# Kernel tuning notes

Hardware: AMD Instinct MI355X
Metric: run time of the kernel (lower is better)

## Reference

```python
import jax, jax.numpy as jnp
import numpy as np

B, S, D, E = 8, 4096, 2048, 8
CHUNK = 128
TAU = 0.7


def setup_inputs() -> dict:
    key = jax.random.key(0)
    k0, k1, k2 = jax.random.split(key, 3)
    H = D // 2
    x = jax.random.normal(k0, (B, S, D), dtype=jnp.float32)
    W1 = jax.random.normal(k1, (D, H), dtype=jnp.float32) * (1.0 / np.sqrt(D))
    b1 = jnp.zeros((H,), dtype=jnp.float32)
    W2 = jax.random.normal(k2, (H, E), dtype=jnp.float32) * (1.0 / np.sqrt(H))
    b2 = jnp.zeros((E,), dtype=jnp.float32)
    return {"x": x, "W1": W1, "b1": b1, "W2": W2, "b2": b2}


def reference(x, W1, b1, W2, b2):
    b, s, d = x.shape
    e = W2.shape[1]
    c = s // CHUNK  # num_chunks (seq_len divisible by chunk_size)
    # router MLP: Linear -> ReLU -> Linear
    logits = jnp.maximum(x @ W1 + b1, 0.0) @ W2 + b2  # [B,S,E]
    # per-chunk mean logits
    chunk_logits = logits.reshape(b, c, CHUNK, e).mean(axis=2)  # [B,C,E]
    bidx = jnp.arange(b)
    # chunk 0: plain argmax
    init = jnp.argmax(chunk_logits[:, 0], axis=-1)  # [B]
    # chunks 1..C-1: hysteresis recurrence via scan
    def step(prev, cl):  # cl: [B,E]
        ce = jnp.argmax(cl, axis=-1)
        diff = cl[bidx, ce] - cl[bidx, prev]
        new = jnp.where(diff > TAU, ce, prev)
        return new, new
    _, rest = jax.lax.scan(step, init, jnp.swapaxes(chunk_logits[:, 1:], 0, 1))
    expert_indices = jnp.concatenate([init[:, None], rest.T], axis=1)  # [B,C]
    oh = jax.nn.one_hot(expert_indices, e, dtype=logits.dtype)  # [B,C,E]
    routing_weights = jnp.broadcast_to(oh[:, :, None, :], (b, c, CHUNK, e)).reshape(b, s, e)
    return routing_weights, expert_indices
```

## Files before the change

kernel.cpp:

```cpp
#include <hip/hip_runtime.h>

typedef unsigned int uint;
typedef unsigned short ushort;

#define BB 8
#define SS 4096
#define DD 2048
#define HH 1024
#define EE 8
#define CHUNK 128
#define NCHUNK 32
#define TAU 0.7f

#define BM 128
#define BN 128
#define BK 32
#define KITERS (DD / BK)

typedef short bf16x8 __attribute__((ext_vector_type(8)));
typedef float f32x16 __attribute__((ext_vector_type(16)));

__device__ inline uint pack_hi(float a, float b) {
    return (__float_as_uint(a) >> 16) | (__float_as_uint(b) & 0xFFFF0000u);
}
__device__ inline float hi_part(float a) {
    return __uint_as_float(__float_as_uint(a) & 0xFFFF0000u);
}

__global__ __launch_bounds__(256) void reorder_w1_kernel(
    const float* __restrict__ W1, ushort* __restrict__ w1hi, ushort* __restrict__ w1lo)
{
    const int kg = blockIdx.x >> 2;
    const int n  = ((blockIdx.x & 3) << 8) + threadIdx.x;
    float v[8];
#pragma unroll
    for (int j = 0; j < 8; ++j) v[j] = W1[(size_t)(kg * 8 + j) * HH + n];
    uint hi[4], lo[4];
#pragma unroll
    for (int p = 0; p < 4; ++p) {
        const float a = v[2 * p], b = v[2 * p + 1];
        hi[p] = pack_hi(a, b);
        lo[p] = pack_hi(a - hi_part(a), b - hi_part(b));
    }
    const size_t off = (size_t)kg * HH + n;
    ((uint4*)w1hi)[off] = make_uint4(hi[0], hi[1], hi[2], hi[3]);
    ((uint4*)w1lo)[off] = make_uint4(lo[0], lo[1], lo[2], lo[3]);
}

__global__ __launch_bounds__(256, 2) void router_gemm_kernel(
    const float* __restrict__ x,
    const ushort* __restrict__ w1hi,
    const ushort* __restrict__ w1lo,
    const float* __restrict__ b1,
    const float* __restrict__ W2,
    float* __restrict__ chunk_logits)
{
    const int slice = blockIdx.x;
    const int bc    = blockIdx.y;
    const int n0    = slice * BN;

    const int tid  = threadIdx.x;
    const int wave = tid >> 6;
    const int lane = tid & 63;
    const int lm   = lane & 31;
    const int kq   = lane >> 5;
    const int wm   = (wave & 1) * 64;
    const int wn   = (wave >> 1) * 64;

    __shared__ ushort As_hi[4][BM][8];
    __shared__ ushort As_lo[4][BM][8];
    __shared__ ushort Bs_hi[4][BN][8];
    __shared__ ushort Bs_lo[4][BN][8];
    __shared__ float  W2s[BN][EE];
    __shared__ float  b1s[BN];
    __shared__ float  red[4][EE];

    const float* xrow = x + (size_t)bc * CHUNK * DD;

    ((float4*)&W2s[0][0])[tid] = ((const float4*)(W2 + (size_t)n0 * EE))[tid];
    if (tid < BN / 4) ((float4*)b1s)[tid] = ((const float4*)(b1 + n0))[tid];

    f32x16 acc[2][2];
#pragma unroll
    for (int i = 0; i < 2; ++i)
#pragma unroll
        for (int j = 0; j < 2; ++j)
#pragma unroll
            for (int r = 0; r < 16; ++r) acc[i][j][r] = 0.0f;

    const int am = tid >> 1;
    const int ah = tid & 1;

    for (int it = 0; it < KITERS; ++it) {
        const int k0 = it * BK;
        __syncthreads();

        {
            const int kgg = (k0 >> 3) + wave;
#pragma unroll
            for (int h = 0; h < 2; ++h) {
                const size_t goff = ((size_t)kgg * HH + n0 + h * 64 + lane) * 8;
                __builtin_amdgcn_global_load_lds(
                    (const __attribute__((address_space(1))) uint*)(w1hi + goff),
                    (__attribute__((address_space(3))) uint*)&Bs_hi[wave][h * 64 + lane][0],
                    16, 0, 0);
                __builtin_amdgcn_global_load_lds(
                    (const __attribute__((address_space(1))) uint*)(w1lo + goff),
                    (__attribute__((address_space(3))) uint*)&Bs_lo[wave][h * 64 + lane][0],
                    16, 0, 0);
            }
        }

        {
            const float* src = xrow + (size_t)am * DD + k0 + ah * 16;
            float4 v0 = ((const float4*)src)[0];
            float4 v1 = ((const float4*)src)[1];
            float4 v2 = ((const float4*)src)[2];
            float4 v3 = ((const float4*)src)[3];
            const float f[16] = {v0.x, v0.y, v0.z, v0.w, v1.x, v1.y, v1.z, v1.w,
                                 v2.x, v2.y, v2.z, v2.w, v3.x, v3.y, v3.z, v3.w};
            uint hi[8], lo[8];
#pragma unroll
            for (int p = 0; p < 8; ++p) {
                const float a = f[2 * p], b = f[2 * p + 1];
                hi[p] = pack_hi(a, b);
                lo[p] = pack_hi(a - hi_part(a), b - hi_part(b));
            }
            const int kg0 = ah * 2;
            *(uint4*)&As_hi[kg0][am][0]     = make_uint4(hi[0], hi[1], hi[2], hi[3]);
            *(uint4*)&As_hi[kg0 + 1][am][0] = make_uint4(hi[4], hi[5], hi[6], hi[7]);
            *(uint4*)&As_lo[kg0][am][0]     = make_uint4(lo[0], lo[1], lo[2], lo[3]);
            *(uint4*)&As_lo[kg0 + 1][am][0] = make_uint4(lo[4], lo[5], lo[6], lo[7]);
        }

        __syncthreads();

#pragma unroll
        for (int s = 0; s < 2; ++s) {
            const int kg = 2 * s + kq;
            bf16x8 a_h[2], a_l[2], b_h[2], b_l[2];
#pragma unroll
            for (int i = 0; i < 2; ++i) {
                a_h[i] = *(const bf16x8*)&As_hi[kg][wm + i * 32 + lm][0];
                a_l[i] = *(const bf16x8*)&As_lo[kg][wm + i * 32 + lm][0];
            }
#pragma unroll
            for (int j = 0; j < 2; ++j) {
                b_h[j] = *(const bf16x8*)&Bs_hi[kg][wn + j * 32 + lm][0];
                b_l[j] = *(const bf16x8*)&Bs_lo[kg][wn + j * 32 + lm][0];
            }
#pragma unroll
            for (int i = 0; i < 2; ++i)
#pragma unroll
                for (int j = 0; j < 2; ++j) {
                    acc[i][j] = __builtin_amdgcn_mfma_f32_32x32x16_bf16(
                        a_l[i], b_h[j], acc[i][j], 0, 0, 0);
                    acc[i][j] = __builtin_amdgcn_mfma_f32_32x32x16_bf16(
                        a_h[i], b_l[j], acc[i][j], 0, 0, 0);
                    acc[i][j] = __builtin_amdgcn_mfma_f32_32x32x16_bf16(
                        a_h[i], b_h[j], acc[i][j], 0, 0, 0);
                }
        }
    }

    float part[EE];
#pragma unroll
    for (int e = 0; e < EE; ++e) part[e] = 0.0f;

#pragma unroll
    for (int j = 0; j < 2; ++j) {
        const int hl = wn + j * 32 + lm;
        const float bias = b1s[hl];
        float w2r[EE];
#pragma unroll
        for (int e = 0; e < EE; ++e) w2r[e] = W2s[hl][e];
#pragma unroll
        for (int i = 0; i < 2; ++i)
#pragma unroll
            for (int r = 0; r < 16; ++r) {
                const float hv = fmaxf(acc[i][j][r] + bias, 0.0f);
#pragma unroll
                for (int e = 0; e < EE; ++e) part[e] = fmaf(hv, w2r[e], part[e]);
            }
    }

#pragma unroll
    for (int off = 32; off >= 1; off >>= 1)
#pragma unroll
        for (int e = 0; e < EE; ++e) part[e] += __shfl_down(part[e], off, 64);

    if (lane == 0)
#pragma unroll
        for (int e = 0; e < EE; ++e) red[wave][e] = part[e];
    __syncthreads();
    if (tid < EE) {
        const float s = red[0][tid] + red[1][tid] + red[2][tid] + red[3][tid];
        atomicAdd(&chunk_logits[(size_t)bc * EE + tid], s * (1.0f / CHUNK));
    }
}

__global__ void hysteresis_kernel(const float* __restrict__ chunk_logits,
                                  const float* __restrict__ b2,
                                  int* __restrict__ eidx_ws,
                                  float* __restrict__ out_idx)
{
    __shared__ float cls[BB * NCHUNK * EE];
    const int tid = threadIdx.x;
#pragma unroll
    for (int i = 0; i < 8; ++i)
        ((float4*)cls)[tid + i * 64] = ((const float4*)chunk_logits)[tid + i * 64];
    __syncthreads();

    const int b = tid;
    if (b >= BB) return;
    float b2r[EE];
#pragma unroll
    for (int e = 0; e < EE; ++e) b2r[e] = b2[e];

    const float* cl = cls + b * NCHUNK * EE;
    int prev = 0;
    for (int c = 0; c < NCHUNK; ++c) {
        float v[EE];
        float best = -3.4e38f;
        int ce = 0;
#pragma unroll
        for (int e = 0; e < EE; ++e) {
            const float lv = cl[c * EE + e] + b2r[e];
            v[e] = lv;
            if (lv > best) { best = lv; ce = e; }
        }
        if (c == 0) prev = ce;
        else if (best - v[prev] > TAU) prev = ce;
        eidx_ws[b * NCHUNK + c] = prev;
        out_idx[b * NCHUNK + c] = (float)prev;
    }
}

__global__ __launch_bounds__(256) void onehot_kernel(const int* __restrict__ eidx,
                                                     float* __restrict__ out)
{
    const int tok = blockIdx.x * blockDim.x + threadIdx.x;
    if (tok >= BB * SS) return;
    const int b = tok / SS;
    const int s = tok - b * SS;
    const int idx = eidx[b * NCHUNK + (s / CHUNK)];
    float vals[EE];
#pragma unroll
    for (int e = 0; e < EE; ++e) vals[e] = (e == idx) ? 1.0f : 0.0f;
    float4* o = (float4*)(out + (size_t)tok * EE);
    o[0] = make_float4(vals[0], vals[1], vals[2], vals[3]);
    o[1] = make_float4(vals[4], vals[5], vals[6], vals[7]);
}

extern "C" void kernel_launch(void* const* d_in, const int* in_sizes, int n_in,
                              void* d_out, int out_size, void* d_ws, size_t ws_size,
                              hipStream_t stream)
{
    const float* x  = (const float*)d_in[0];
    const float* W1 = (const float*)d_in[1];
    const float* b1 = (const float*)d_in[2];
    const float* W2 = (const float*)d_in[3];
    const float* b2 = (const float*)d_in[4];
    float* out = (float*)d_out;

    ushort* w1hi        = (ushort*)d_ws;
    ushort* w1lo        = (ushort*)((char*)d_ws + (size_t)4 * 1024 * 1024);
    float*  chunk_logits = (float*)((char*)d_ws + (size_t)8 * 1024 * 1024);
    int*    eidx        = (int*)((char*)d_ws + (size_t)8 * 1024 * 1024 + 8192);

    hipMemsetAsync(chunk_logits, 0, BB * NCHUNK * EE * sizeof(float), stream);

    reorder_w1_kernel<<<1024, 256, 0, stream>>>(W1, w1hi, w1lo);

    dim3 grid(HH / BN, BB * NCHUNK);
    router_gemm_kernel<<<grid, 256, 0, stream>>>(x, w1hi, w1lo, b1, W2, chunk_logits);

    hysteresis_kernel<<<1, 64, 0, stream>>>(chunk_logits, b2, eidx,
                                            out + (size_t)BB * SS * EE);

    onehot_kernel<<<(BB * SS + 255) / 256, 256, 0, stream>>>(eidx, out);
}
```

Baseline: 695.4 us.

## Double-buffer LDS tiles to overlap global loads with MFMA compute

The GEMM main loop now keeps two LDS buffers for the A and B tiles. The next K-slice's W1 async global-to-LDS loads and x register loads are issued before the MFMAs on the current buffer, and the split A tile is written after them. This cuts one of the two barriers per iteration and is meant to hide global memory latency behind matrix math. In exchange it doubles LDS use for the tiles (32KB total), which may limit occupancy, and it keeps 16 more floats live in registers across the MFMA phase.

```diff
diff --git a/kernel.cpp b/kernel.cpp
--- a/kernel.cpp
+++ b/kernel.cpp
@@ -67,10 +67,10 @@
     const int wm   = (wave & 1) * 64;
     const int wn   = (wave >> 1) * 64;
 
-    __shared__ ushort As_hi[4][BM][8];
-    __shared__ ushort As_lo[4][BM][8];
-    __shared__ ushort Bs_hi[4][BN][8];
-    __shared__ ushort Bs_lo[4][BN][8];
+    __shared__ __align__(16) ushort As_hi[2][4][BM][8];
+    __shared__ __align__(16) ushort As_lo[2][4][BM][8];
+    __shared__ __align__(16) ushort Bs_hi[2][4][BN][8];
+    __shared__ __align__(16) ushort Bs_lo[2][4][BN][8];
     __shared__ float  W2s[BN][EE];
     __shared__ float  b1s[BN];
     __shared__ float  red[4][EE];
@@ -90,78 +90,93 @@
 
     const int am = tid >> 1;
     const int ah = tid & 1;
-
-    for (int it = 0; it < KITERS; ++it) {
-        const int k0 = it * BK;
+    const float* asrc = xrow + (size_t)am * DD + ah * 16;
+
+#define STAGE_B(it, buf) do {                                                        \
+        const int kgg = (it) * 4 + wave;                                             \
+        _Pragma("unroll")                                                            \
+        for (int h = 0; h < 2; ++h) {                                                \
+            const size_t goff = ((size_t)kgg * HH + n0 + h * 64 + lane) * 8;         \
+            __builtin_amdgcn_global_load_lds(                                        \
+                (const __attribute__((address_space(1))) uint*)(w1hi + goff),        \
+                (__attribute__((address_space(3))) uint*)&Bs_hi[buf][wave][h * 64 + lane][0], \
+                16, 0, 0);                                                           \
+            __builtin_amdgcn_global_load_lds(                                        \
+                (const __attribute__((address_space(1))) uint*)(w1lo + goff),        \
+                (__attribute__((address_space(3))) uint*)&Bs_lo[buf][wave][h * 64 + lane][0], \
+                16, 0, 0);                                                           \
+        }                                                                            \
+    } while (0)
+
+#define WRITE_A(v0, v1, v2, v3, buf) do {                                            \
+        const float f_[16] = {v0.x, v0.y, v0.z, v0.w, v1.x, v1.y, v1.z, v1.w,        \
+                              v2.x, v2.y, v2.z, v2.w, v3.x, v3.y, v3.z, v3.w};       \
+        uint h_[8], l_[8];                                                           \
+        _Pragma("unroll")                                                            \
+        for (int p = 0; p < 8; ++p) {                                                \
+            const float a_ = f_[2 * p], b_ = f_[2 * p + 1];                          \
+            h_[p] = pack_hi(a_, b_);                                                 \
+            l_[p] = pack_hi(a_ - hi_part(a_), b_ - hi_part(b_));                     \
+        }                                                                            \
+        const int kg0_ = ah * 2;                                                     \
+        *(uint4*)&As_hi[buf][kg0_][am][0]     = make_uint4(h_[0], h_[1], h_[2], h_[3]); \
+        *(uint4*)&As_hi[buf][kg0_ + 1][am][0] = make_uint4(h_[4], h_[5], h_[6], h_[7]); \
+        *(uint4*)&As_lo[buf][kg0_][am][0]     = make_uint4(l_[0], l_[1], l_[2], l_[3]); \
+        *(uint4*)&As_lo[buf][kg0_ + 1][am][0] = make_uint4(l_[4], l_[5], l_[6], l_[7]); \
+    } while (0)
+
+#define MFMA_PHASE(buf) do {                                                         \
+        _Pragma("unroll")                                                            \
+        for (int s = 0; s < 2; ++s) {                                                \
+            const int kg = 2 * s + kq;                                               \
+            bf16x8 a_h[2], a_l[2], b_h[2], b_l[2];                                   \
+            _Pragma("unroll")                                                        \
+            for (int i = 0; i < 2; ++i) {                                            \
+                a_h[i] = *(const bf16x8*)&As_hi[buf][kg][wm + i * 32 + lm][0];       \
+                a_l[i] = *(const bf16x8*)&As_lo[buf][kg][wm + i * 32 + lm][0];       \
+            }                                                                        \
+            _Pragma("unroll")                                                        \
+            for (int j = 0; j < 2; ++j) {                                            \
+                b_h[j] = *(const bf16x8*)&Bs_hi[buf][kg][wn + j * 32 + lm][0];       \
+                b_l[j] = *(const bf16x8*)&Bs_lo[buf][kg][wn + j * 32 + lm][0];       \
+            }                                                                        \
+            _Pragma("unroll")                                                        \
+            for (int i = 0; i < 2; ++i)                                              \
+                _Pragma("unroll")                                                    \
+                for (int j = 0; j < 2; ++j) {                                        \
+                    acc[i][j] = __builtin_amdgcn_mfma_f32_32x32x16_bf16(             \
+                        a_l[i], b_h[j], acc[i][j], 0, 0, 0);                         \
+                    acc[i][j] = __builtin_amdgcn_mfma_f32_32x32x16_bf16(             \
+                        a_h[i], b_l[j], acc[i][j], 0, 0, 0);                         \
+                    acc[i][j] = __builtin_amdgcn_mfma_f32_32x32x16_bf16(             \
+                        a_h[i], b_h[j], acc[i][j], 0, 0, 0);                         \
+                }                                                                    \
+        }                                                                            \
+    } while (0)
+
+    {
+        float4 v0 = ((const float4*)asrc)[0];
+        float4 v1 = ((const float4*)asrc)[1];
+        float4 v2 = ((const float4*)asrc)[2];
+        float4 v3 = ((const float4*)asrc)[3];
+        STAGE_B(0, 0);
+        WRITE_A(v0, v1, v2, v3, 0);
+    }
+    __syncthreads();
+
+    for (int t = 0; t < KITERS - 1; ++t) {
+        const int cur = t & 1;
+        const float* s2 = asrc + (size_t)(t + 1) * BK;
+        float4 v0 = ((const float4*)s2)[0];
+        float4 v1 = ((const float4*)s2)[1];
+        float4 v2 = ((const float4*)s2)[2];
+        float4 v3 = ((const float4*)s2)[3];
+        STAGE_B(t + 1, cur ^ 1);
+        MFMA_PHASE(cur);
+        WRITE_A(v0, v1, v2, v3, cur ^ 1);
         __syncthreads();
-
-        {
-            const int kgg = (k0 >> 3) + wave;
-#pragma unroll
-            for (int h = 0; h < 2; ++h) {
-                const size_t goff = ((size_t)kgg * HH + n0 + h * 64 + lane) * 8;
-                __builtin_amdgcn_global_load_lds(
-                    (const __attribute__((address_space(1))) uint*)(w1hi + goff),
-                    (__attribute__((address_space(3))) uint*)&Bs_hi[wave][h * 64 + lane][0],
-                    16, 0, 0);
-                __builtin_amdgcn_global_load_lds(
-                    (const __attribute__((address_space(1))) uint*)(w1lo + goff),
-                    (__attribute__((address_space(3))) uint*)&Bs_lo[wave][h * 64 + lane][0],
-                    16, 0, 0);
-            }
-        }
-
-        {
-            const float* src = xrow + (size_t)am * DD + k0 + ah * 16;
-            float4 v0 = ((const float4*)src)[0];
-            float4 v1 = ((const float4*)src)[1];
-            float4 v2 = ((const float4*)src)[2];
-            float4 v3 = ((const float4*)src)[3];
-            const float f[16] = {v0.x, v0.y, v0.z, v0.w, v1.x, v1.y, v1.z, v1.w,
-                                 v2.x, v2.y, v2.z, v2.w, v3.x, v3.y, v3.z, v3.w};
-            uint hi[8], lo[8];
-#pragma unroll
-            for (int p = 0; p < 8; ++p) {
-                const float a = f[2 * p], b = f[2 * p + 1];
-                hi[p] = pack_hi(a, b);
-                lo[p] = pack_hi(a - hi_part(a), b - hi_part(b));
-            }
-            const int kg0 = ah * 2;
-            *(uint4*)&As_hi[kg0][am][0]     = make_uint4(hi[0], hi[1], hi[2], hi[3]);
-            *(uint4*)&As_hi[kg0 + 1][am][0] = make_uint4(hi[4], hi[5], hi[6], hi[7]);
-            *(uint4*)&As_lo[kg0][am][0]     = make_uint4(lo[0], lo[1], lo[2], lo[3]);
-            *(uint4*)&As_lo[kg0 + 1][am][0] = make_uint4(lo[4], lo[5], lo[6], lo[7]);
-        }
-
-        __syncthreads();
-
-#pragma unroll
-        for (int s = 0; s < 2; ++s) {
-            const int kg = 2 * s + kq;
-            bf16x8 a_h[2], a_l[2], b_h[2], b_l[2];
-#pragma unroll
-            for (int i = 0; i < 2; ++i) {
-                a_h[i] = *(const bf16x8*)&As_hi[kg][wm + i * 32 + lm][0];
-                a_l[i] = *(const bf16x8*)&As_lo[kg][wm + i * 32 + lm][0];
-            }
-#pragma unroll
-            for (int j = 0; j < 2; ++j) {
-                b_h[j] = *(const bf16x8*)&Bs_hi[kg][wn + j * 32 + lm][0];
-                b_l[j] = *(const bf16x8*)&Bs_lo[kg][wn + j * 32 + lm][0];
-            }
-#pragma unroll
-            for (int i = 0; i < 2; ++i)
-#pragma unroll
-                for (int j = 0; j < 2; ++j) {
-                    acc[i][j] = __builtin_amdgcn_mfma_f32_32x32x16_bf16(
-                        a_l[i], b_h[j], acc[i][j], 0, 0, 0);
-                    acc[i][j] = __builtin_amdgcn_mfma_f32_32x32x16_bf16(
-                        a_h[i], b_l[j], acc[i][j], 0, 0, 0);
-                    acc[i][j] = __builtin_amdgcn_mfma_f32_32x32x16_bf16(
-                        a_h[i], b_h[j], acc[i][j], 0, 0, 0);
-                }
-        }
-    }
+    }
+    MFMA_PHASE((KITERS - 1) & 1);
 
     float part[EE];
 #pragma unroll
@@ -263,10 +278,10 @@
     const float* b2 = (const float*)d_in[4];
     float* out = (float*)d_out;
 
-    ushort* w1hi        = (ushort*)d_ws;
-    ushort* w1lo        = (ushort*)((char*)d_ws + (size_t)4 * 1024 * 1024);
+    ushort* w1hi         = (ushort*)d_ws;
+    ushort* w1lo         = (ushort*)((char*)d_ws + (size_t)4 * 1024 * 1024);
     float*  chunk_logits = (float*)((char*)d_ws + (size_t)8 * 1024 * 1024);
-    int*    eidx        = (int*)((char*)d_ws + (size_t)8 * 1024 * 1024 + 8192);
+    int*    eidx         = (int*)((char*)d_ws + (size_t)8 * 1024 * 1024 + 8192);
 
     hipMemsetAsync(chunk_logits, 0, BB * NCHUNK * EE * sizeof(float), stream);
 
```

Result: slower. 894.6 us (+28.6%).
